# Kernel tuning notes

Hardware: AMD Instinct MI355X
Metric: run time of the kernel (lower is better)

Reference implementation:

```python
import jax, jax.numpy as jnp
import numpy as np
import math

B, S, D, H = 64, 575, 256, 8
FF = 4 * D
EPS = 1e-5
DILATIONS = (1, 2, 4)


def _ln(x, g, b):
    mu = jnp.mean(x, axis=-1, keepdims=True)
    var = jnp.var(x, axis=-1, keepdims=True)
    return (x - mu) * jax.lax.rsqrt(var + EPS) * g + b


def setup_inputs() -> dict:
    key = jax.random.key(0)
    ks = jax.random.split(key, 8)
    w = lambda k, shape: jax.random.normal(k, shape, jnp.float32) * 0.02
    return {
        'state': jax.random.normal(ks[0], (B, S, D), jnp.float32),
        'conv_w': w(ks[1], (3, D, D, 3, 3)),
        'conv_b': jnp.zeros((3, D), jnp.float32),
        'qkv_w': w(ks[2], (3 * D, D)),
        'qkv_b': jnp.zeros((3 * D,), jnp.float32),
        'o_w': w(ks[3], (D, D)),
        'o_b': jnp.zeros((D,), jnp.float32),
        'attn_bias': w(ks[4], (H, S, S)),
        'ffp_w': w(ks[5], (FF, D)),
        'ffp_b': jnp.zeros((FF,), jnp.float32),
        'ffg_w': w(ks[6], (FF, D)),
        'ffg_b': jnp.zeros((FF,), jnp.float32),
        'ffo_w': w(ks[7], (D, FF)),
        'ffo_b': jnp.zeros((D,), jnp.float32),
        'n1_g': jnp.ones((D,), jnp.float32), 'n1_b': jnp.zeros((D,), jnp.float32),
        'n2_g': jnp.ones((D,), jnp.float32), 'n2_b': jnp.zeros((D,), jnp.float32),
        'n3_g': jnp.ones((D,), jnp.float32), 'n3_b': jnp.zeros((D,), jnp.float32),
    }


def _forward(state, conv_w, conv_b, qkv_w, qkv_b, o_w, o_b, attn_bias,
             ffp_w, ffp_b, ffg_w, ffg_b, ffo_w, ffo_b,
             n1_g, n1_b, n2_g, n2_b, n3_g, n3_b):
    b, s, d = state.shape
    h = attn_bias.shape[0]
    hd = d // h
    spatial = int(round(math.sqrt(s + 1)))  # grid_size + 1; spatial^2 == s+1 here

    # --- multi-scale dilated conv mixing ---
    pad = jnp.zeros((b, 1, d), state.dtype)
    h2d = jnp.concatenate([pad, state], axis=1)            # (B, S+1, D)
    h2d = jnp.transpose(h2d, (0, 2, 1)).reshape(b, d, spatial, spatial)
    conv_sum = 0.0
    for i, dil in enumerate(DILATIONS):
        y = jax.lax.conv_general_dilated(
            h2d, conv_w[i], window_strides=(1, 1),
            padding=[(dil, dil), (dil, dil)], rhs_dilation=(dil, dil),
            dimension_numbers=('NCHW', 'OIHW', 'NCHW'))
        conv_sum = conv_sum + y + conv_b[i][None, :, None, None]
    h_flat = jnp.transpose(conv_sum.reshape(b, d, -1), (0, 2, 1))  # (B, S+1, D)
    hmix = h_flat[:, 1:, :]

    state = _ln(state + hmix, n1_g, n1_b)

    # --- self-attention with learned per-head pair bias ---
    qkv = state @ qkv_w.T + qkv_b                          # (B, S, 3D)
    q, k, v = jnp.split(qkv, 3, axis=-1)
    # NOTE: replicate torch's reshape (no transpose): (B,S,D) -> (B,H,S,hd)
    q = q.reshape(b, h, s, hd)
    k = k.reshape(b, h, s, hd)
    v = v.reshape(b, h, s, hd)
    scores = jnp.einsum('bhsd,bhtd->bhst', q, k) / math.sqrt(hd)
    scores = scores + attn_bias[None]
    attn = jax.nn.softmax(scores, axis=-1)
    out = jnp.einsum('bhst,bhtd->bhsd', attn, v)
    out = jnp.transpose(out, (0, 2, 1, 3)).reshape(b, s, d)

    state = _ln(state + out @ o_w.T + o_b, n2_g, n2_b)

    # --- gated feed-forward ---
    proj = state @ ffp_w.T + ffp_b
    gate = jax.nn.sigmoid(state @ ffg_w.T + ffg_b)
    ff = (proj * gate) @ ffo_w.T + ffo_b
    return _ln(state + ff, n3_g, n3_b)


def reference(state, conv_w, conv_b, qkv_w, qkv_b, o_w, o_b, attn_bias,
              ffp_w, ffp_b, ffg_w, ffg_b, ffo_w, ffo_b,
              n1_g, n1_b, n2_g, n2_b, n3_g, n3_b):
    return _forward(state, conv_w, conv_b, qkv_w, qkv_b, o_w, o_b, attn_bias,
                    ffp_w, ffp_b, ffg_w, ffg_b, ffo_w, ffo_b,
                    n1_g, n1_b, n2_g, n2_b, n3_g, n3_b)
```

## Files before the change

kernel.cpp:

```cpp
#include <hip/hip_runtime.h>
#include <hip/hip_bf16.h>
#include <cstdio>


typedef __attribute__((ext_vector_type(8))) short s8v;
typedef __attribute__((ext_vector_type(4))) float f32x4;
typedef unsigned short u16;

constexpr int kB = 64, kS = 575, kD = 256, kH = 8, kP = 576, kFF = 1024;
constexpr int kRows = kB * kS;
constexpr float kEps = 1e-5f;
constexpr float kScale = 0.17677669529663687f;
constexpr size_t kPdStride = 9420800;

__device__ __forceinline__ u16 f2b(float f) {
  __hip_bfloat16 h = __float2bfloat16(f);
  return *reinterpret_cast<u16*>(&h);
}
__device__ __forceinline__ void unpack2(unsigned int w, float& lo, float& hi) {
  union { float f; unsigned int u; } a, b;
  a.u = w << 16;
  b.u = w & 0xffff0000u;
  lo = a.f;
  hi = b.f;
}

__device__ __forceinline__ void gll16(const void* g, void* l) {
  __builtin_amdgcn_global_load_lds((const __attribute__((address_space(1))) void*)g,
                                   (__attribute__((address_space(3))) void*)l, 16, 0, 0);
}

__global__ void k_pack_convw(const float* __restrict__ cw, u16* __restrict__ wc) {
  int idx = blockIdx.x * 256 + threadIdx.x;
  if (idx >= 27 * kD * kD) return;
  int ci = idx & 255;
  int co = (idx >> 8) & 255;
  int tap = idx >> 16;
  int i = tap / 9, r = tap - i * 9;
  int ky = r / 3, kx = r - ky * 3;
  wc[idx] = f2b(cw[(((size_t)(i * kD + co) * kD + ci) * 3 + ky) * 3 + kx]);
}

__global__ void k_tobf16(const float* __restrict__ in, u16* __restrict__ out, int n) {
  int i = blockIdx.x * 256 + threadIdx.x;
  if (i < n) out[i] = f2b(in[i]);
}

__global__ void k_make_x0(const float* __restrict__ state, u16* __restrict__ x0,
                          u16* __restrict__ zrow) {
  int bp = blockIdx.x;
  int c = threadIdx.x;
  if (bp == kB * kP) { zrow[c] = 0; return; }
  int p = bp % kP;
  int b = bp / kP;
  float v = (p == 0) ? 0.f : state[((size_t)(b * kS + p - 1)) * kD + c];
  x0[(size_t)bp * kD + c] = f2b(v);
}

__global__ __launch_bounds__(256) void k_gemm(const u16* __restrict__ A,
                                              const u16* __restrict__ Bw,
                                              const float* __restrict__ bias,
                                              u16* __restrict__ Cb,
                                              int M, int N, int K) {
  __shared__ u16 As[2][8192];
  __shared__ u16 Bs[2][8192];
  const int t = threadIdx.x;
  const int wave = t >> 6, lane = t & 63;
  const int wm = wave >> 1, wn = wave & 1;
  const int lr = lane & 15, lk = lane >> 4;
  const int m0 = blockIdx.x * 128, n0 = blockIdx.y * 128;
  const int lrow = lane >> 3;
  const int swzk = ((lane & 7) ^ lrow) * 8;
  const u16 *ga[4], *gb[4];
#pragma unroll
  for (int i = 0; i < 4; ++i) {
    int r = 8 * wave + lrow + 32 * i;
    int ra = m0 + r;
    if (ra > M - 1) ra = M - 1;
    ga[i] = A + (size_t)ra * K + swzk;
    gb[i] = Bw + (size_t)(n0 + r) * K + swzk;
  }
  auto stage = [&](int kt, int buf) {
#pragma unroll
    for (int i = 0; i < 4; ++i) {
      gll16(ga[i] + kt, &As[buf][i * 2048 + wave * 512]);
      gll16(gb[i] + kt, &Bs[buf][i * 2048 + wave * 512]);
    }
  };
  f32x4 acc[4][4] = {};
  stage(0, 0);
  __syncthreads();
  const int NT = K >> 6;
  for (int s = 0; s < NT; ++s) {
    const int cur = s & 1;
    if (s + 1 < NT) stage((s + 1) << 6, cur ^ 1);
    s8v af[2][4], bfr[2][4];
#pragma unroll
    for (int kk = 0; kk < 2; ++kk)
#pragma unroll
      for (int i = 0; i < 4; ++i) {
        const int rA = wm * 64 + i * 16 + lr;
        const int rB = wn * 64 + i * 16 + lr;
        af[kk][i] = *(const s8v*)(&As[cur][rA * 64 + ((kk * 32 + lk * 8) ^ ((rA & 7) << 3))]);
        bfr[kk][i] = *(const s8v*)(&Bs[cur][rB * 64 + ((kk * 32 + lk * 8) ^ ((rB & 7) << 3))]);
      }
#pragma unroll
    for (int kk = 0; kk < 2; ++kk)
#pragma unroll
      for (int i = 0; i < 4; ++i)
#pragma unroll
        for (int j = 0; j < 4; ++j)
          acc[i][j] = __builtin_amdgcn_mfma_f32_16x16x32_bf16(af[kk][i], bfr[kk][j], acc[i][j], 0, 0, 0);
    __syncthreads();
  }
#pragma unroll
  for (int i = 0; i < 4; ++i) {
    const int rbase = m0 + wm * 64 + i * 16 + lk * 4;
#pragma unroll
    for (int j = 0; j < 4; ++j) {
      const int col = n0 + wn * 64 + j * 16 + lr;
      const float bv = bias[col];
#pragma unroll
      for (int q = 0; q < 4; ++q) {
        int r = rbase + q;
        if (r < M) Cb[(size_t)r * N + col] = f2b(acc[i][j][q] + bv);
      }
    }
  }
}

__global__ __launch_bounds__(256) void k_ff1(const u16* __restrict__ A,
                                             const u16* __restrict__ Wf,
                                             const float* __restrict__ pb,
                                             const float* __restrict__ gb,
                                             u16* __restrict__ H, int M) {
  __shared__ u16 As[4096];
  __shared__ u16 Bp[4096];
  __shared__ u16 Bg[4096];
  const int t = threadIdx.x;
  const int wave = t >> 6;
  const int wm = wave >> 1, wn = wave & 1;
  const int lr = threadIdx.x & 15, lk = (threadIdx.x & 63) >> 4;
  const int m0 = blockIdx.x * 128, n0 = blockIdx.y * 128;
  int ra = m0 + (t >> 2);
  int rb = ra + 64;
  if (ra > M - 1) ra = M - 1;
  if (rb > M - 1) rb = M - 1;
  const int koff = (t & 3) * 8;
  const u16* gA0 = A + (size_t)ra * kD + koff;
  const u16* gA1 = A + (size_t)rb * kD + koff;
  const u16* gP0 = Wf + (size_t)(n0 + (t >> 2)) * kD + koff;
  const u16* gP1 = gP0 + (size_t)64 * kD;
  const u16* gG0 = gP0 + (size_t)1024 * kD;
  const u16* gG1 = gP1 + (size_t)1024 * kD;
  u16* lA0 = As + wave * 512;
  u16* lA1 = As + 2048 + wave * 512;
  u16* lP0 = Bp + wave * 512;
  u16* lP1 = Bp + 2048 + wave * 512;
  u16* lG0 = Bg + wave * 512;
  u16* lG1 = Bg + 2048 + wave * 512;
  f32x4 ap[4][4] = {};
  f32x4 ag[4][4] = {};
  for (int kt = 0; kt < kD; kt += 32) {
    gll16(gA0 + kt, lA0);
    gll16(gA1 + kt, lA1);
    gll16(gP0 + kt, lP0);
    gll16(gP1 + kt, lP1);
    gll16(gG0 + kt, lG0);
    gll16(gG1 + kt, lG1);
    __syncthreads();
    s8v af[4], bp4[4], bg4[4];
#pragma unroll
    for (int i = 0; i < 4; ++i) {
      af[i] = *(const s8v*)(As + (wm * 64 + i * 16 + lr) * 32 + lk * 8);
      bp4[i] = *(const s8v*)(Bp + (wn * 64 + i * 16 + lr) * 32 + lk * 8);
      bg4[i] = *(const s8v*)(Bg + (wn * 64 + i * 16 + lr) * 32 + lk * 8);
    }
#pragma unroll
    for (int i = 0; i < 4; ++i)
#pragma unroll
      for (int j = 0; j < 4; ++j) {
        ap[i][j] = __builtin_amdgcn_mfma_f32_16x16x32_bf16(af[i], bp4[j], ap[i][j], 0, 0, 0);
        ag[i][j] = __builtin_amdgcn_mfma_f32_16x16x32_bf16(af[i], bg4[j], ag[i][j], 0, 0, 0);
      }
    __syncthreads();
  }
#pragma unroll
  for (int i = 0; i < 4; ++i) {
    const int rbase = m0 + wm * 64 + i * 16 + lk * 4;
#pragma unroll
    for (int j = 0; j < 4; ++j) {
      const int col = n0 + wn * 64 + j * 16 + lr;
      const float pbv = pb[col], gbv = gb[col];
#pragma unroll
      for (int q = 0; q < 4; ++q) {
        int r = rbase + q;
        if (r < M) {
          float p = ap[i][j][q] + pbv;
          float g = ag[i][j][q] + gbv;
          H[(size_t)r * kFF + col] = f2b(p * (1.f / (1.f + __expf(-g))));
        }
      }
    }
  }
}

__global__ __launch_bounds__(256) void k_conv(const u16* __restrict__ X0,
                                              const u16* __restrict__ zrow,
                                              const u16* __restrict__ Wc,
                                              const float* __restrict__ cb,
                                              u16* __restrict__ pd) {
  __shared__ u16 As[2][8192];
  __shared__ u16 Bs[2][8192];
  const int t = threadIdx.x;
  const int wave = t >> 6, lane = t & 63;
  const int wm = wave >> 1, wn = wave & 1;
  const int lr = lane & 15, lk = lane >> 4;
  const int m0 = blockIdx.x * 128;
  const int n0 = blockIdx.y * 128;
  const int di = blockIdx.z;
  const int dil = 1 << di;
  const int lrow = lane >> 3;
  const int swzk = ((lane & 7) ^ lrow) * 8;
  const u16* Wd = Wc + (size_t)di * 9 * (kD * kD);
  int bb[4], py[4], px[4];
  const u16* gw[4];
#pragma unroll
  for (int i = 0; i < 4; ++i) {
    int r = 8 * wave + lrow + 32 * i;
    int m = m0 + r;
    bb[i] = m / 576;
    int p = m - bb[i] * 576;
    py[i] = p / 24;
    px[i] = p - py[i] * 24;
    gw[i] = Wd + (size_t)(n0 + r) * kD + swzk;
  }
  auto stage = [&](int s, int buf) {
    const int tap = s >> 2, kc = (s & 3) << 6;
    const int dy = (tap / 3 - 1) * dil;
    const int dx = (tap % 3 - 1) * dil;
#pragma unroll
    for (int i = 0; i < 4; ++i) {
      const int ny = py[i] + dy, nx = px[i] + dx;
      const bool v = ((unsigned)ny < 24u) & ((unsigned)nx < 24u);
      const u16* sa = v ? X0 + (((size_t)(bb[i] * kP + ny * 24 + nx)) << 8) + kc + swzk
                        : zrow + swzk;
      gll16(sa, &As[buf][i * 2048 + wave * 512]);
      gll16(gw[i] + (size_t)tap * (kD * kD) + kc, &Bs[buf][i * 2048 + wave * 512]);
    }
  };
  f32x4 acc[4][4] = {};
  stage(0, 0);
  __syncthreads();
  for (int s = 0; s < 36; ++s) {
    const int cur = s & 1;
    if (s < 35) stage(s + 1, cur ^ 1);
    s8v af[2][4], bfr[2][4];
#pragma unroll
    for (int kk = 0; kk < 2; ++kk)
#pragma unroll
      for (int ii = 0; ii < 4; ++ii) {
        const int rA = wm * 64 + ii * 16 + lr;
        const int rB = wn * 64 + ii * 16 + lr;
        af[kk][ii] = *(const s8v*)(&As[cur][rA * 64 + ((kk * 32 + lk * 8) ^ ((rA & 7) << 3))]);
        bfr[kk][ii] = *(const s8v*)(&Bs[cur][rB * 64 + ((kk * 32 + lk * 8) ^ ((rB & 7) << 3))]);
      }
#pragma unroll
    for (int kk = 0; kk < 2; ++kk)
#pragma unroll
      for (int ii = 0; ii < 4; ++ii)
#pragma unroll
        for (int jj = 0; jj < 4; ++jj)
          acc[ii][jj] = __builtin_amdgcn_mfma_f32_16x16x32_bf16(af[kk][ii], bfr[kk][jj], acc[ii][jj], 0, 0, 0);
    __syncthreads();
  }
  u16* pdo = pd + (size_t)di * kPdStride;
#pragma unroll
  for (int i2 = 0; i2 < 4; ++i2) {
    const int mbase = m0 + wm * 64 + i2 * 16 + lk * 4;
#pragma unroll
    for (int j = 0; j < 4; ++j) {
      const int col = n0 + wn * 64 + j * 16 + lr;
      const float bv = cb[di * kD + col];
#pragma unroll
      for (int q = 0; q < 4; ++q) {
        const int m = mbase + q;
        const int b2 = m / 576;
        const int p = m - b2 * 576;
        if (p >= 1)
          pdo[((size_t)(b2 * kS + p - 1) << 8) + col] = f2b(acc[i2][j][q] + bv);
      }
    }
  }
}

__global__ __launch_bounds__(256) void k_attn2(const u16* __restrict__ qkv,
                                               const float* __restrict__ bias,
                                               u16* __restrict__ outp) {
  __shared__ u16 KsS[2][2048];
  __shared__ u16 VtS[2][2048];
  __shared__ u16 PsS[4][1024];
  const int qt = blockIdx.x, h = blockIdx.y, b = blockIdx.z;
  const int tid = threadIdx.x;
  const int w = tid >> 6, lane = tid & 63;
  const int lg = lane >> 4, lr = lane & 15;
  const int q0 = qt * 64;
  const int qrow_a = q0 + w * 16 + lr;
  const int qrow_ac = qrow_a < kS ? qrow_a : kS - 1;
  s8v qf;
  {
    int F = h * (kS * 32) + qrow_ac * 32 + lg * 8;
    qf = *(const s8v*)(qkv + ((size_t)(b * kS + (F >> 8))) * 768 + (F & 255));
  }
  const int trel = tid >> 2;
  const int dcol = (tid & 3) * 8;
  float mrun[4], lsum[4];
#pragma unroll
  for (int r = 0; r < 4; ++r) { mrun[r] = -1e30f; lsum[r] = 0.f; }
  f32x4 o0 = {0.f, 0.f, 0.f, 0.f}, o1 = {0.f, 0.f, 0.f, 0.f};
  const f32x4 zf = {0.f, 0.f, 0.f, 0.f};
  const int qrow_s = q0 + w * 16 + lg * 4;
  const size_t kvrowbase = (size_t)(b * kS) * 768;

  for (int kt = 0; kt < 9; ++kt) {
    const int t0 = kt * 64;
    const int buf = kt & 1;
    {
      const int tg = t0 + trel;
      const bool tv = tg < kS;
      const int tcl = tv ? tg : kS - 1;
      const int Fk = h * (kS * 32) + tcl * 32 + dcol;
      const u16* kp = qkv + kvrowbase + (size_t)(Fk >> 8) * 768 + 256 + (Fk & 255);
      uint4 kd = {0, 0, 0, 0}, vd = {0, 0, 0, 0};
      if (tv) {
        kd = *(const uint4*)kp;
        vd = *(const uint4*)(kp + 256);
      }
      *(uint4*)&KsS[buf][trel * 32 + (dcol ^ ((trel & 3) << 3))] = kd;
      union { uint4 u4; u16 us[8]; } vu;
      vu.u4 = vd;
#pragma unroll
      for (int j = 0; j < 8; ++j) {
        const int d = dcol + j;
        VtS[buf][d * 64 + (trel ^ ((d & 7) << 3))] = vu.us[j];
      }
    }
    float bv[4][4];
#pragma unroll
    for (int r = 0; r < 4; ++r) {
      const int qr = qrow_s + r;
      const float* bp = bias + ((size_t)h * kS + (qr < kS ? qr : kS - 1)) * kS;
#pragma unroll
      for (int j = 0; j < 4; ++j) {
        const int tg = t0 + j * 16 + lr;
        bv[j][r] = (tg < kS) ? bp[tg] : -1e30f;
      }
    }
    __syncthreads();
    f32x4 sc[4];
#pragma unroll
    for (int j = 0; j < 4; ++j) {
      const int krow = j * 16 + lr;
      s8v kf = *(const s8v*)&KsS[buf][krow * 32 + ((lg * 8) ^ ((krow & 3) << 3))];
      sc[j] = __builtin_amdgcn_mfma_f32_16x16x32_bf16(qf, kf, zf, 0, 0, 0);
    }
#pragma unroll
    for (int r = 0; r < 4; ++r) {
      float s4[4];
      float sm = -1e30f;
#pragma unroll
      for (int j = 0; j < 4; ++j) {
        s4[j] = fmaf(sc[j][r], kScale, bv[j][r]);
        sm = fmaxf(sm, s4[j]);
      }
      sm = fmaxf(sm, __shfl_xor(sm, 1));
      sm = fmaxf(sm, __shfl_xor(sm, 2));
      sm = fmaxf(sm, __shfl_xor(sm, 4));
      sm = fmaxf(sm, __shfl_xor(sm, 8));
      const float nm = fmaxf(mrun[r], sm);
      const float corr = __expf(mrun[r] - nm);
      mrun[r] = nm;
      float psum = 0.f;
      const int prow = lg * 4 + r;
#pragma unroll
      for (int j = 0; j < 4; ++j) {
        const float p = __expf(s4[j] - nm);
        psum += p;
        PsS[w][prow * 64 + ((j * 16 + lr) ^ ((prow & 7) << 3))] = f2b(p);
      }
      lsum[r] = fmaf(lsum[r], corr, psum);
      o0[r] *= corr;
      o1[r] *= corr;
    }
#pragma unroll
    for (int c = 0; c < 2; ++c) {
      const int pcol = c * 32 + lg * 8;
      s8v pf = *(const s8v*)&PsS[w][lr * 64 + (pcol ^ ((lr & 7) << 3))];
      s8v vf0 = *(const s8v*)&VtS[buf][lr * 64 + (pcol ^ ((lr & 7) << 3))];
      s8v vf1 = *(const s8v*)&VtS[buf][(16 + lr) * 64 + (pcol ^ (((16 + lr) & 7) << 3))];
      o0 = __builtin_amdgcn_mfma_f32_16x16x32_bf16(pf, vf0, o0, 0, 0, 0);
      o1 = __builtin_amdgcn_mfma_f32_16x16x32_bf16(pf, vf1, o1, 0, 0, 0);
    }
  }
#pragma unroll
  for (int r = 0; r < 4; ++r) {
    float lt = lsum[r];
    lt += __shfl_xor(lt, 1);
    lt += __shfl_xor(lt, 2);
    lt += __shfl_xor(lt, 4);
    lt += __shfl_xor(lt, 8);
    const float inv = 1.f / lt;
    const int qr = qrow_s + r;
    if (qr < kS) {
      u16* op = outp + ((size_t)(b * kS + qr)) * kD + h * 32;
      op[lr] = f2b(o0[r] * inv);
      op[16 + lr] = f2b(o1[r] * inv);
    }
  }
}

__global__ __launch_bounds__(256) void k_add_ln(const float* __restrict__ xa,
                                                const u16* __restrict__ xb,
                                                const float* __restrict__ g,
                                                const float* __restrict__ be,
                                                float* __restrict__ of, u16* __restrict__ ob) {
  const int wave = threadIdx.x >> 6, lane = threadIdx.x & 63;
  const int row = blockIdx.x * 4 + wave;
  const float4 a = ((const float4*)(xa + (size_t)row * kD))[lane];
  uint2 bw = ((const uint2*)(xb + (size_t)row * kD))[lane];
  float b0, b1, b2, b3;
  unpack2(bw.x, b0, b1);
  unpack2(bw.y, b2, b3);
  float x0 = a.x + b0, x1 = a.y + b1, x2 = a.z + b2, x3 = a.w + b3;
  float sum = x0 + x1 + x2 + x3;
  float sq = fmaf(x0, x0, fmaf(x1, x1, fmaf(x2, x2, x3 * x3)));
  for (int off = 1; off < 64; off <<= 1) {
    sum += __shfl_xor(sum, off);
    sq += __shfl_xor(sq, off);
  }
  const float mean = sum * (1.f / 256.f);
  const float var = sq * (1.f / 256.f) - mean * mean;
  const float rs = rsqrtf(var + kEps);
  const float4 gg = ((const float4*)g)[lane];
  const float4 bt = ((const float4*)be)[lane];
  float y0 = (x0 - mean) * rs * gg.x + bt.x;
  float y1 = (x1 - mean) * rs * gg.y + bt.y;
  float y2 = (x2 - mean) * rs * gg.z + bt.z;
  float y3 = (x3 - mean) * rs * gg.w + bt.w;
  float4 yo = {y0, y1, y2, y3};
  ((float4*)(of + (size_t)row * kD))[lane] = yo;
  if (ob) {
    u16* po = ob + (size_t)row * kD + lane * 4;
    po[0] = f2b(y0); po[1] = f2b(y1); po[2] = f2b(y2); po[3] = f2b(y3);
  }
}

__global__ __launch_bounds__(256) void k_add_ln3(const float* __restrict__ xa,
                                                 const u16* __restrict__ pa,
                                                 const u16* __restrict__ pbq,
                                                 const u16* __restrict__ pc,
                                                 const float* __restrict__ g,
                                                 const float* __restrict__ be,
                                                 float* __restrict__ of, u16* __restrict__ ob) {
  const int wave = threadIdx.x >> 6, lane = threadIdx.x & 63;
  const int row = blockIdx.x * 4 + wave;
  const size_t base = (size_t)row * kD;
  const float4 a = ((const float4*)(xa + base))[lane];
  uint2 w0 = ((const uint2*)(pa + base))[lane];
  uint2 w1 = ((const uint2*)(pbq + base))[lane];
  uint2 w2 = ((const uint2*)(pc + base))[lane];
  float a0, a1, a2, a3, c0, c1, c2, c3, d0, d1, d2, d3;
  unpack2(w0.x, a0, a1); unpack2(w0.y, a2, a3);
  unpack2(w1.x, c0, c1); unpack2(w1.y, c2, c3);
  unpack2(w2.x, d0, d1); unpack2(w2.y, d2, d3);
  float x0 = a.x + a0 + c0 + d0, x1 = a.y + a1 + c1 + d1;
  float x2 = a.z + a2 + c2 + d2, x3 = a.w + a3 + c3 + d3;
  float sum = x0 + x1 + x2 + x3;
  float sq = fmaf(x0, x0, fmaf(x1, x1, fmaf(x2, x2, x3 * x3)));
  for (int off = 1; off < 64; off <<= 1) {
    sum += __shfl_xor(sum, off);
    sq += __shfl_xor(sq, off);
  }
  const float mean = sum * (1.f / 256.f);
  const float var = sq * (1.f / 256.f) - mean * mean;
  const float rs = rsqrtf(var + kEps);
  const float4 gg = ((const float4*)g)[lane];
  const float4 bt = ((const float4*)be)[lane];
  float y0 = (x0 - mean) * rs * gg.x + bt.x;
  float y1 = (x1 - mean) * rs * gg.y + bt.y;
  float y2 = (x2 - mean) * rs * gg.z + bt.z;
  float y3 = (x3 - mean) * rs * gg.w + bt.w;
  float4 yo = {y0, y1, y2, y3};
  ((float4*)(of + base))[lane] = yo;
  u16* po = ob + base + lane * 4;
  po[0] = f2b(y0); po[1] = f2b(y1); po[2] = f2b(y2); po[3] = f2b(y3);
}

extern "C" void kernel_launch(void* const* d_in, const int* in_sizes, int n_in,
                              void* d_out, int out_size, void* d_ws, size_t ws_size,
                              hipStream_t stream) {
  const float* state = (const float*)d_in[0];
  const float* conv_w = (const float*)d_in[1];
  const float* conv_b = (const float*)d_in[2];
  const float* qkv_w = (const float*)d_in[3];
  const float* qkv_b = (const float*)d_in[4];
  const float* o_w = (const float*)d_in[5];
  const float* o_b = (const float*)d_in[6];
  const float* attn_bias = (const float*)d_in[7];
  const float* ffp_w = (const float*)d_in[8];
  const float* ffp_b = (const float*)d_in[9];
  const float* ffg_w = (const float*)d_in[10];
  const float* ffg_b = (const float*)d_in[11];
  const float* ffo_w = (const float*)d_in[12];
  const float* ffo_b = (const float*)d_in[13];
  const float* n1_g = (const float*)d_in[14];
  const float* n1_b = (const float*)d_in[15];
  const float* n2_g = (const float*)d_in[16];
  const float* n2_b = (const float*)d_in[17];
  const float* n3_g = (const float*)d_in[18];
  const float* n3_b = (const float*)d_in[19];

  constexpr size_t kWsNeed = 137527296;
  if (ws_size < kWsNeed) {
    fprintf(stderr, "[kernel] ws_size=%zu < need=%zu\n", ws_size, kWsNeed);
    return;
  }
  char* ws = (char*)d_ws;
  u16* Wc = (u16*)(ws + 0);
  u16* Wqkv = (u16*)(ws + 3538944);
  u16* Wo = (u16*)(ws + 3932160);
  u16* Wff = (u16*)(ws + 4063232);
  u16* Wffo = (u16*)(ws + 5111808);
  float* stF = (float*)(ws + 5636096);
  u16* stB = (u16*)(ws + 43319296);
  char* S4 = ws + 62160896;
  u16* X0 = (u16*)(ws + 5636096);
  u16* zrow = (u16*)(ws + 43319296);
  u16* pd = (u16*)S4;
  u16* qkvb = (u16*)S4;
  u16* attnout = (u16*)(S4 + 56524800);
  u16* oprojb = (u16*)S4;
  u16* ffh = (u16*)S4;
  float* outp = (float*)d_out;

  k_pack_convw<<<6912, 256, 0, stream>>>(conv_w, Wc);
  k_tobf16<<<768, 256, 0, stream>>>(qkv_w, Wqkv, 768 * 256);
  k_tobf16<<<256, 256, 0, stream>>>(o_w, Wo, 256 * 256);
  k_tobf16<<<1024, 256, 0, stream>>>(ffp_w, Wff, 1024 * 256);
  k_tobf16<<<1024, 256, 0, stream>>>(ffg_w, Wff + 1024 * 256, 1024 * 256);
  k_tobf16<<<1024, 256, 0, stream>>>(ffo_w, Wffo, 256 * 1024);
  k_make_x0<<<kB * kP + 1, 256, 0, stream>>>(state, X0, zrow);

  k_conv<<<dim3(288, 2, 3), 256, 0, stream>>>(X0, zrow, Wc, conv_b, pd);
  k_add_ln3<<<kRows / 4, 256, 0, stream>>>(state, pd, pd + kPdStride, pd + 2 * kPdStride,
                                           n1_g, n1_b, stF, stB);

  k_gemm<<<dim3(288, 6), 256, 0, stream>>>(stB, Wqkv, qkv_b, qkvb, kRows, 768, 256);
  k_attn2<<<dim3(9, kH, kB), 256, 0, stream>>>(qkvb, attn_bias, attnout);
  k_gemm<<<dim3(288, 2), 256, 0, stream>>>(attnout, Wo, o_b, oprojb, kRows, 256, 256);
  k_add_ln<<<kRows / 4, 256, 0, stream>>>(stF, oprojb, n2_g, n2_b, stF, stB);

  k_ff1<<<dim3(288, 8), 256, 0, stream>>>(stB, Wff, ffp_b, ffg_b, ffh, kRows);
  k_gemm<<<dim3(288, 2), 256, 0, stream>>>(ffh, Wffo, ffo_b, stB, kRows, 256, 1024);
  k_add_ln<<<kRows / 4, 256, 0, stream>>>(stF, stB, n3_g, n3_b, outp, nullptr);
}
```

Measured before the change: 612.7 us.

## Double-buffer and swizzle FF1 LDS tiles; restructure conv staging per tap

The gated FF1 GEMM kernel now double-buffers its A/proj/gate LDS tiles so the next K-slice's global-to-LDS loads overlap the current MFMA work. Its LDS layout also gets an XOR swizzle on the K offset to cut bank conflicts. The conv kernel's staging loop is split into per-tap and per-channel-chunk loops, with source row pointers precomputed once per tap instead of recomputing bounds and addresses on every stage. The cost is doubled LDS use in FF1 (48KB), which may lower occupancy.

```diff
diff --git a/kernel.cpp b/kernel.cpp
--- a/kernel.cpp
+++ b/kernel.cpp
@@ -134,47 +134,50 @@
                                              const float* __restrict__ pb,
                                              const float* __restrict__ gb,
                                              u16* __restrict__ H, int M) {
-  __shared__ u16 As[4096];
-  __shared__ u16 Bp[4096];
-  __shared__ u16 Bg[4096];
+  __shared__ u16 As[2][4096];
+  __shared__ u16 Bp[2][4096];
+  __shared__ u16 Bg[2][4096];
   const int t = threadIdx.x;
   const int wave = t >> 6;
   const int wm = wave >> 1, wn = wave & 1;
-  const int lr = threadIdx.x & 15, lk = (threadIdx.x & 63) >> 4;
+  const int lr = t & 15, lk = (t & 63) >> 4;
   const int m0 = blockIdx.x * 128, n0 = blockIdx.y * 128;
   int ra = m0 + (t >> 2);
   int rb = ra + 64;
   if (ra > M - 1) ra = M - 1;
   if (rb > M - 1) rb = M - 1;
-  const int koff = (t & 3) * 8;
+  const int koff = (((t & 3) ^ ((t >> 2) & 3)) * 8);
   const u16* gA0 = A + (size_t)ra * kD + koff;
   const u16* gA1 = A + (size_t)rb * kD + koff;
   const u16* gP0 = Wf + (size_t)(n0 + (t >> 2)) * kD + koff;
   const u16* gP1 = gP0 + (size_t)64 * kD;
   const u16* gG0 = gP0 + (size_t)1024 * kD;
   const u16* gG1 = gP1 + (size_t)1024 * kD;
-  u16* lA0 = As + wave * 512;
-  u16* lA1 = As + 2048 + wave * 512;
-  u16* lP0 = Bp + wave * 512;
-  u16* lP1 = Bp + 2048 + wave * 512;
-  u16* lG0 = Bg + wave * 512;
-  u16* lG1 = Bg + 2048 + wave * 512;
+  auto stage = [&](int kt, int buf) {
+    gll16(gA0 + kt, &As[buf][wave * 512]);
+    gll16(gA1 + kt, &As[buf][2048 + wave * 512]);
+    gll16(gP0 + kt, &Bp[buf][wave * 512]);
+    gll16(gP1 + kt, &Bp[buf][2048 + wave * 512]);
+    gll16(gG0 + kt, &Bg[buf][wave * 512]);
+    gll16(gG1 + kt, &Bg[buf][2048 + wave * 512]);
+  };
   f32x4 ap[4][4] = {};
   f32x4 ag[4][4] = {};
-  for (int kt = 0; kt < kD; kt += 32) {
-    gll16(gA0 + kt, lA0);
-    gll16(gA1 + kt, lA1);
-    gll16(gP0 + kt, lP0);
-    gll16(gP1 + kt, lP1);
-    gll16(gG0 + kt, lG0);
-    gll16(gG1 + kt, lG1);
-    __syncthreads();
+  stage(0, 0);
+  __syncthreads();
+  for (int s = 0; s < 8; ++s) {
+    const int cur = s & 1;
+    if (s < 7) stage((s + 1) << 5, cur ^ 1);
     s8v af[4], bp4[4], bg4[4];
 #pragma unroll
     for (int i = 0; i < 4; ++i) {
-      af[i] = *(const s8v*)(As + (wm * 64 + i * 16 + lr) * 32 + lk * 8);
-      bp4[i] = *(const s8v*)(Bp + (wn * 64 + i * 16 + lr) * 32 + lk * 8);
-      bg4[i] = *(const s8v*)(Bg + (wn * 64 + i * 16 + lr) * 32 + lk * 8);
+      const int rA = wm * 64 + i * 16 + lr;
+      const int rB = wn * 64 + i * 16 + lr;
+      const int oA = rA * 32 + ((lk * 8) ^ ((rA & 3) << 3));
+      const int oB = rB * 32 + ((lk * 8) ^ ((rB & 3) << 3));
+      af[i] = *(const s8v*)(&As[cur][oA]);
+      bp4[i] = *(const s8v*)(&Bp[cur][oB]);
+      bg4[i] = *(const s8v*)(&Bg[cur][oB]);
     }
 #pragma unroll
     for (int i = 0; i < 4; ++i)
@@ -222,57 +225,74 @@
   const int dil = 1 << di;
   const int lrow = lane >> 3;
   const int swzk = ((lane & 7) ^ lrow) * 8;
-  const u16* Wd = Wc + (size_t)di * 9 * (kD * kD);
-  int bb[4], py[4], px[4];
+  const u16* Wd = Wc + ((size_t)di * 9 << 16);
+  int py[4], px[4];
+  const u16* xrow[4];
   const u16* gw[4];
 #pragma unroll
   for (int i = 0; i < 4; ++i) {
     int r = 8 * wave + lrow + 32 * i;
     int m = m0 + r;
-    bb[i] = m / 576;
-    int p = m - bb[i] * 576;
+    int bbv = m / 576;
+    int p = m - bbv * 576;
     py[i] = p / 24;
     px[i] = p - py[i] * 24;
+    xrow[i] = X0 + (((size_t)(bbv * kP)) << 8) + swzk;
     gw[i] = Wd + (size_t)(n0 + r) * kD + swzk;
   }
-  auto stage = [&](int s, int buf) {
-    const int tap = s >> 2, kc = (s & 3) << 6;
-    const int dy = (tap / 3 - 1) * dil;
-    const int dx = (tap % 3 - 1) * dil;
+  const u16* S0[4];
+  const u16* S1[4];
+  auto csrc = [&](const u16** dst, int dyv, int dxv) {
 #pragma unroll
     for (int i = 0; i < 4; ++i) {
-      const int ny = py[i] + dy, nx = px[i] + dx;
+      const int ny = py[i] + dyv, nx = px[i] + dxv;
       const bool v = ((unsigned)ny < 24u) & ((unsigned)nx < 24u);
-      const u16* sa = v ? X0 + (((size_t)(bb[i] * kP + ny * 24 + nx)) << 8) + kc + swzk
-                        : zrow + swzk;
-      gll16(sa, &As[buf][i * 2048 + wave * 512]);
-      gll16(gw[i] + (size_t)tap * (kD * kD) + kc, &Bs[buf][i * 2048 + wave * 512]);
+      dst[i] = v ? xrow[i] + ((ny * 24 + nx) << 8) : zrow + swzk;
+    }
+  };
+  auto stage = [&](const u16* const* S, size_t woff, int kc, int buf) {
+#pragma unroll
+    for (int i = 0; i < 4; ++i) {
+      gll16(S[i] + kc, &As[buf][i * 2048 + wave * 512]);
+      gll16(gw[i] + woff + kc, &Bs[buf][i * 2048 + wave * 512]);
     }
   };
   f32x4 acc[4][4] = {};
-  stage(0, 0);
+  csrc(S0, -dil, -dil);
+  stage(S0, 0, 0, 0);
   __syncthreads();
-  for (int s = 0; s < 36; ++s) {
-    const int cur = s & 1;
-    if (s < 35) stage(s + 1, cur ^ 1);
-    s8v af[2][4], bfr[2][4];
-#pragma unroll
-    for (int kk = 0; kk < 2; ++kk)
-#pragma unroll
-      for (int ii = 0; ii < 4; ++ii) {
-        const int rA = wm * 64 + ii * 16 + lr;
-        const int rB = wn * 64 + ii * 16 + lr;
-        af[kk][ii] = *(const s8v*)(&As[cur][rA * 64 + ((kk * 32 + lk * 8) ^ ((rA & 7) << 3))]);
-        bfr[kk][ii] = *(const s8v*)(&Bs[cur][rB * 64 + ((kk * 32 + lk * 8) ^ ((rB & 7) << 3))]);
-      }
-#pragma unroll
-    for (int kk = 0; kk < 2; ++kk)
-#pragma unroll
-      for (int ii = 0; ii < 4; ++ii)
-#pragma unroll
-        for (int jj = 0; jj < 4; ++jj)
-          acc[ii][jj] = __builtin_amdgcn_mfma_f32_16x16x32_bf16(af[kk][ii], bfr[kk][jj], acc[ii][jj], 0, 0, 0);
-    __syncthreads();
+  for (int tap = 0; tap < 9; ++tap) {
+    if (tap < 8) {
+      const int tn = tap + 1;
+      csrc(S1, (tn / 3 - 1) * dil, (tn % 3 - 1) * dil);
+    }
+    const size_t woff = (size_t)tap << 16;
+#pragma unroll
+    for (int c = 0; c < 4; ++c) {
+      const int buf = c & 1;
+      if (c < 3) stage(S0, woff, (c + 1) << 6, buf ^ 1);
+      else if (tap < 8) stage(S1, woff + 65536, 0, buf ^ 1);
+      s8v af[2][4], bfr[2][4];
+#pragma unroll
+      for (int kk = 0; kk < 2; ++kk)
+#pragma unroll
+        for (int ii = 0; ii < 4; ++ii) {
+          const int rA = wm * 64 + ii * 16 + lr;
+          const int rB = wn * 64 + ii * 16 + lr;
+          af[kk][ii] = *(const s8v*)(&As[buf][rA * 64 + ((kk * 32 + lk * 8) ^ ((rA & 7) << 3))]);
+          bfr[kk][ii] = *(const s8v*)(&Bs[buf][rB * 64 + ((kk * 32 + lk * 8) ^ ((rB & 7) << 3))]);
+        }
+#pragma unroll
+      for (int kk = 0; kk < 2; ++kk)
+#pragma unroll
+        for (int ii = 0; ii < 4; ++ii)
+#pragma unroll
+          for (int jj = 0; jj < 4; ++jj)
+            acc[ii][jj] = __builtin_amdgcn_mfma_f32_16x16x32_bf16(af[kk][ii], bfr[kk][jj], acc[ii][jj], 0, 0, 0);
+      __syncthreads();
+    }
+#pragma unroll
+    for (int i = 0; i < 4; ++i) S0[i] = S1[i];
   }
   u16* pdo = pd + (size_t)di * kPdStride;
 #pragma unroll
```

Measured after the change: 567.3 us. 7.4% less time.
